# Performance work log

Hardware: AMD Instinct MI355X
Metric: run time of the kernel (lower is better)

Reference implementation:

```python
import jax, jax.numpy as jnp
import numpy as np

B, L = 4096, 200
G_DIM, L_DIM, A_DIM, H = 64, 64, 8, 32
MAX_ACTION = 1.0


def _init(k, shape, fan_in):
    bound = 1.0 / np.sqrt(fan_in)
    return jax.random.uniform(k, shape, jnp.float32, -bound, bound)


def setup_inputs() -> dict:
    key = jax.random.key(0)
    ks = jax.random.split(key, 16)
    return dict(
        global_states=jax.random.normal(ks[0], (B, G_DIM), jnp.float32),
        local_states=jax.random.normal(ks[1], (B, L, L_DIM), jnp.float32),
        W_w=_init(ks[2], (H, G_DIM), G_DIM), W_b=_init(ks[3], (H,), G_DIM),
        U_w=_init(ks[4], (H, L_DIM), L_DIM), U_b=_init(ks[5], (H,), L_DIM),
        att_w=_init(ks[6], (1, 2 * H), 2 * H), att_b=_init(ks[7], (1,), 2 * H),
        l1_w=_init(ks[8], (256, 2 * H), 2 * H), l1_b=_init(ks[9], (256,), 2 * H),
        l2_w=_init(ks[10], (256, 256), 256), l2_b=_init(ks[11], (256,), 256),
        l3_w=_init(ks[12], (A_DIM, 256), 256), l3_b=_init(ks[13], (A_DIM,), 256),
    )


def reference(global_states, local_states, W_w, W_b, U_w, U_b,
              att_w, att_b, l1_w, l1_b, l2_w, l2_b, l3_w, l3_b):
    h = W_w.shape[0]  # 32
    wg = global_states @ W_w.T + W_b                              # [B,H]
    ul = jnp.einsum('bld,hd->blh', local_states, U_w) + U_b       # [B,L,H]
    # att input row0 = cat(wg, wg); rows 1..L = cat(wg, ul)
    a_g, a_l = att_w[0, :h], att_w[0, h:]
    g_term = wg @ a_g                                             # [B]
    s0 = jax.nn.leaky_relu(g_term + wg @ a_l + att_b[0])          # [B]
    sl = jax.nn.leaky_relu(g_term[:, None] + ul @ a_l + att_b[0]) # [B,L]
    # normalize by sum (not softmax), matching torch.div(score, score.sum())
    total = s0 + sl.sum(axis=1)                                   # [B]
    n0 = s0 / total                                               # [B]
    nl = sl / total[:, None]                                      # [B,L]
    agg_local = jnp.einsum('bl,blh->bh', nl, ul)                  # [B,H]
    states = jax.nn.relu(jnp.concatenate([n0[:, None] * wg, agg_local], axis=1))  # [B,2H]
    a = jax.nn.relu(states @ l1_w.T + l1_b)
    a = jax.nn.relu(a @ l2_w.T + l2_b)
    a = jax.nn.sigmoid(a @ l3_w.T + l3_b)
    return MAX_ACTION * a
```

## Files before the change

kernel.cpp:

```cpp
#include <hip/hip_runtime.h>
#include <math.h>

#define BB 4096
#define LL 200
#define HH 32
#define PF 8

__global__ __launch_bounds__(256) void actor_fused_kernel(
    const float* __restrict__ gs,
    const float* __restrict__ ls,
    const float* __restrict__ W_w, const float* __restrict__ W_b,
    const float* __restrict__ U_w, const float* __restrict__ U_b,
    const float* __restrict__ att_w, const float* __restrict__ att_b,
    const float* __restrict__ l1_w, const float* __restrict__ l1_b,
    const float* __restrict__ l2_w, const float* __restrict__ l2_b,
    const float* __restrict__ l3_w, const float* __restrict__ l3_b,
    float* __restrict__ out)
{
    __shared__ float c_lds[4 * 64];
    __shared__ float y_lds[4 * 64];
    __shared__ __align__(16) float s_x [4 * 64];
    __shared__ __align__(16) float s_a1[4 * 256];
    __shared__ __align__(16) float s_a2[4 * 260];

    const int tid  = threadIdx.x;
    const int lane = tid & 63;
    const int wid  = tid >> 6;
    const int b    = blockIdx.x * 4 + wid;

    const int h    = lane & 31;
    const int half = lane >> 5;
    const int q    = lane & 15;
    const int lg   = lane >> 4;


    const float4* g4 = (const float4*)(gs + (size_t)b * 64);
    const float4* W4 = (const float4*)(W_w);
    float wg = (half == 0) ? W_b[h] : 0.f;
    #pragma unroll
    for (int dd = 0; dd < 8; ++dd) {
        float4 gv = g4[half * 8 + dd];
        float4 wv = W4[h * 16 + half * 8 + dd];
        wg += gv.x * wv.x + gv.y * wv.y + gv.z * wv.z + gv.w * wv.w;
    }
    wg += __shfl_xor(wg, 32);

    float gt = wg * att_w[h];
    float t2 = wg * att_w[HH + h];
    #pragma unroll
    for (int m = 1; m < 32; m <<= 1) {
        gt += __shfl_xor(gt, m);
        t2 += __shfl_xor(t2, m);
    }
    const float attb = att_b[0];
    const float lin0 = gt + t2 + attb;
    const float s0   = (lin0 > 0.f) ? lin0 : 0.01f * lin0;

    float c = 0.f;
    float ubal = 0.f;
    #pragma unroll
    for (int hh = 0; hh < HH; ++hh) {
        const float alh = att_w[HH + hh];
        c    += alh * U_w[hh * 64 + lane];
        ubal += alh * U_b[hh];
    }
    c_lds[wid * 64 + lane] = c;
    __syncthreads();
    const float4 cq = *(const float4*)&c_lds[wid * 64 + 4 * q];
    const float base = gt + ubal + attb;

    const float4* xs = (const float4*)(ls + (size_t)b * (LL * 64));
    const int idx0 = lg * 16 + q;
    float4 yx = make_float4(0.f, 0.f, 0.f, 0.f);
    float Sacc = 0.f;

    float4 Xbuf[PF];
    #pragma unroll
    for (int i = 0; i < PF; ++i)
        Xbuf[i] = xs[idx0 + i * 64];

    #pragma unroll
    for (int t = 0; t < 50; ++t) {
        float4 X = Xbuf[t & (PF - 1)];
        int tn = t + PF;
        if (tn > 49) tn = 49;
        Xbuf[t & (PF - 1)] = xs[idx0 + tn * 64];

        float p = X.x * cq.x + X.y * cq.y + X.z * cq.z + X.w * cq.w;
        p += __shfl_xor(p, 1);
        p += __shfl_xor(p, 2);
        p += __shfl_xor(p, 4);
        p += __shfl_xor(p, 8);
        const float linv = p + base;
        const float sl = (linv > 0.f) ? linv : 0.01f * linv;
        yx.x += sl * X.x;
        yx.y += sl * X.y;
        yx.z += sl * X.z;
        yx.w += sl * X.w;
        Sacc += sl;
    }

    #pragma unroll
    for (int m = 16; m < 64; m <<= 1) {
        yx.x += __shfl_xor(yx.x, m);
        yx.y += __shfl_xor(yx.y, m);
        yx.z += __shfl_xor(yx.z, m);
        yx.w += __shfl_xor(yx.w, m);
        Sacc += __shfl_xor(Sacc, m);
    }
    if (lane < 16) *(float4*)&y_lds[wid * 64 + 4 * q] = yx;
    __syncthreads();

    float V = (half == 0) ? (U_b[h] * Sacc) : 0.f;
    const float4* U4 = (const float4*)U_w;
    const float4* y4 = (const float4*)&y_lds[wid * 64];
    #pragma unroll
    for (int dd = 0; dd < 8; ++dd) {
        float4 uv = U4[h * 16 + half * 8 + dd];
        float4 yv = y4[half * 8 + dd];
        V += uv.x * yv.x + uv.y * yv.y + uv.z * yv.z + uv.w * yv.w;
    }
    V += __shfl_xor(V, 32);

    const float total = s0 + Sacc;
    const float n0    = s0 / total;
    const float outv  = (lane < 32) ? (n0 * wg) : (V / total);
    s_x[wid * 64 + lane] = fmaxf(outv, 0.f);
    __syncthreads();


    float w[64];

    {
        const float* wr = l1_w + tid * 64;
        #pragma unroll
        for (int d = 0; d < 64; ++d) w[d] = wr[d];
        float bias = l1_b[tid];
        #pragma unroll
        for (int r = 0; r < 4; ++r) {
            float acc = bias;
            #pragma unroll
            for (int d = 0; d < 64; ++d)
                acc += s_x[r * 64 + d] * w[d];
            s_a1[r * 256 + tid] = fmaxf(acc, 0.f);
        }
    }
    __syncthreads();

    {
        float acc[4];
        float bias = l2_b[tid];
        #pragma unroll
        for (int r = 0; r < 4; ++r) acc[r] = bias;
        for (int kc = 0; kc < 4; ++kc) {
            const float* wr = l2_w + tid * 256 + kc * 64;
            #pragma unroll
            for (int d = 0; d < 64; ++d) w[d] = wr[d];
            #pragma unroll
            for (int r = 0; r < 4; ++r) {
                #pragma unroll
                for (int d = 0; d < 64; ++d)
                    acc[r] += s_a1[r * 256 + kc * 64 + d] * w[d];
            }
        }
        #pragma unroll
        for (int r = 0; r < 4; ++r)
            s_a2[r * 260 + tid] = fmaxf(acc[r], 0.f);
    }
    __syncthreads();

    if (tid < 32) {
        int r = tid >> 3, o = tid & 7;
        float acc = l3_b[o];
        const float4* wr4 = (const float4*)(l3_w + o * 256);
        const float4* a4  = (const float4*)&s_a2[r * 260];
        #pragma unroll 8
        for (int k = 0; k < 64; ++k) {
            float4 av = a4[k];
            float4 wv = wr4[k];
            acc += av.x * wv.x + av.y * wv.y + av.z * wv.z + av.w * wv.w;
        }
        out[(size_t)(blockIdx.x * 4 + r) * 8 + o] =
            1.f / (1.f + __expf(-acc));
    }
}

extern "C" void kernel_launch(void* const* d_in, const int* in_sizes, int n_in,
                              void* d_out, int out_size, void* d_ws, size_t ws_size,
                              hipStream_t stream)
{
    const float* gs    = (const float*)d_in[0];
    const float* ls    = (const float*)d_in[1];
    const float* W_w   = (const float*)d_in[2];
    const float* W_b   = (const float*)d_in[3];
    const float* U_w   = (const float*)d_in[4];
    const float* U_b   = (const float*)d_in[5];
    const float* att_w = (const float*)d_in[6];
    const float* att_b = (const float*)d_in[7];
    const float* l1_w  = (const float*)d_in[8];
    const float* l1_b  = (const float*)d_in[9];
    const float* l2_w  = (const float*)d_in[10];
    const float* l2_b  = (const float*)d_in[11];
    const float* l3_w  = (const float*)d_in[12];
    const float* l3_b  = (const float*)d_in[13];

    actor_fused_kernel<<<BB / 4, 256, 0, stream>>>(
        gs, ls, W_w, W_b, U_w, U_b, att_w, att_b,
        l1_w, l1_b, l2_w, l2_b, l3_w, l3_b, (float*)d_out);
}
```

Before: 354.5 us.

## Process 16 batch rows per block to amortize MLP weight loads

Each block now handles 16 batch rows with 1024 threads instead of 4 rows with 256, so each l1/l2 weight row is loaded once per 16 rows rather than per 4. This cuts cache and memory traffic for the MLP weights. The MLP stages now use float4 weight and activation loads, and the shared c vector is stored once per block. In exchange, only 256 of the 1024 threads work during the MLP stages and there are far fewer blocks, which may underfill the GPU. The larger per-thread accumulators under the tightened launch bounds may also cause register spills.

```diff
diff --git a/kernel.cpp b/kernel.cpp
--- a/kernel.cpp
+++ b/kernel.cpp
@@ -5,8 +5,10 @@
 #define LL 200
 #define HH 32
 #define PF 8
-
-__global__ __launch_bounds__(256) void actor_fused_kernel(
+#define ROWS 16
+
+
+__global__ __launch_bounds__(1024, 4) void actor_fused_kernel(
     const float* __restrict__ gs,
     const float* __restrict__ ls,
     const float* __restrict__ W_w, const float* __restrict__ W_b,
@@ -17,21 +19,20 @@
     const float* __restrict__ l3_w, const float* __restrict__ l3_b,
     float* __restrict__ out)
 {
-    __shared__ float c_lds[4 * 64];
-    __shared__ float y_lds[4 * 64];
-    __shared__ __align__(16) float s_x [4 * 64];
-    __shared__ __align__(16) float s_a1[4 * 256];
-    __shared__ __align__(16) float s_a2[4 * 260];
+    __shared__ float c_lds[64];
+    __shared__ __align__(16) float y_lds[ROWS][64];
+    __shared__ __align__(16) float s_x [ROWS * 64];
+    __shared__ __align__(16) float s_a1[ROWS * 260];
+    __shared__ __align__(16) float s_a2[ROWS * 260];
 
     const int tid  = threadIdx.x;
     const int lane = tid & 63;
     const int wid  = tid >> 6;
-    const int b    = blockIdx.x * 4 + wid;
+    const int b    = blockIdx.x * ROWS + wid;
 
     const int h    = lane & 31;
     const int half = lane >> 5;
     const int q    = lane & 15;
-    const int lg   = lane >> 4;
 
 
     const float4* g4 = (const float4*)(gs + (size_t)b * 64);
@@ -64,27 +65,26 @@
         c    += alh * U_w[hh * 64 + lane];
         ubal += alh * U_b[hh];
     }
-    c_lds[wid * 64 + lane] = c;
-    __syncthreads();
-    const float4 cq = *(const float4*)&c_lds[wid * 64 + 4 * q];
+    c_lds[lane] = c;
+    __syncthreads();
+    const float4 cq = *(const float4*)&c_lds[4 * q];
     const float base = gt + ubal + attb;
 
     const float4* xs = (const float4*)(ls + (size_t)b * (LL * 64));
-    const int idx0 = lg * 16 + q;
     float4 yx = make_float4(0.f, 0.f, 0.f, 0.f);
     float Sacc = 0.f;
 
     float4 Xbuf[PF];
     #pragma unroll
     for (int i = 0; i < PF; ++i)
-        Xbuf[i] = xs[idx0 + i * 64];
+        Xbuf[i] = xs[lane + i * 64];
 
     #pragma unroll
     for (int t = 0; t < 50; ++t) {
         float4 X = Xbuf[t & (PF - 1)];
         int tn = t + PF;
         if (tn > 49) tn = 49;
-        Xbuf[t & (PF - 1)] = xs[idx0 + tn * 64];
+        Xbuf[t & (PF - 1)] = xs[lane + tn * 64];
 
         float p = X.x * cq.x + X.y * cq.y + X.z * cq.z + X.w * cq.w;
         p += __shfl_xor(p, 1);
@@ -108,12 +108,12 @@
         yx.w += __shfl_xor(yx.w, m);
         Sacc += __shfl_xor(Sacc, m);
     }
-    if (lane < 16) *(float4*)&y_lds[wid * 64 + 4 * q] = yx;
+    if (lane < 16) *(float4*)&y_lds[wid][4 * q] = yx;
     __syncthreads();
 
     float V = (half == 0) ? (U_b[h] * Sacc) : 0.f;
     const float4* U4 = (const float4*)U_w;
-    const float4* y4 = (const float4*)&y_lds[wid * 64];
+    const float4* y4 = (const float4*)&y_lds[wid][0];
     #pragma unroll
     for (int dd = 0; dd < 8; ++dd) {
         float4 uv = U4[h * 16 + half * 8 + dd];
@@ -128,59 +128,70 @@
     s_x[wid * 64 + lane] = fmaxf(outv, 0.f);
     __syncthreads();
 
-
-    float w[64];
-
-    {
-        const float* wr = l1_w + tid * 64;
-        #pragma unroll
-        for (int d = 0; d < 64; ++d) w[d] = wr[d];
-        float bias = l1_b[tid];
-        #pragma unroll
-        for (int r = 0; r < 4; ++r) {
-            float acc = bias;
+    const int u = tid & 255;
+
+    if (tid < 256) {
+        float4 wv[16];
+        const float4* wr4 = (const float4*)(l1_w + u * 64);
+        #pragma unroll
+        for (int i = 0; i < 16; ++i) wv[i] = wr4[i];
+        float acc[ROWS];
+        const float bias = l1_b[u];
+        #pragma unroll
+        for (int r = 0; r < ROWS; ++r) acc[r] = bias;
+        #pragma unroll
+        for (int i = 0; i < 16; ++i) {
+            const float4 w4v = wv[i];
             #pragma unroll
-            for (int d = 0; d < 64; ++d)
-                acc += s_x[r * 64 + d] * w[d];
-            s_a1[r * 256 + tid] = fmaxf(acc, 0.f);
-        }
-    }
-    __syncthreads();
-
-    {
-        float acc[4];
-        float bias = l2_b[tid];
-        #pragma unroll
-        for (int r = 0; r < 4; ++r) acc[r] = bias;
-        for (int kc = 0; kc < 4; ++kc) {
-            const float* wr = l2_w + tid * 256 + kc * 64;
-            #pragma unroll
-            for (int d = 0; d < 64; ++d) w[d] = wr[d];
-            #pragma unroll
-            for (int r = 0; r < 4; ++r) {
-                #pragma unroll
-                for (int d = 0; d < 64; ++d)
-                    acc[r] += s_a1[r * 256 + kc * 64 + d] * w[d];
+            for (int r = 0; r < ROWS; ++r) {
+                const float4 xv = *(const float4*)&s_x[r * 64 + i * 4];
+                acc[r] += w4v.x * xv.x + w4v.y * xv.y + w4v.z * xv.z + w4v.w * xv.w;
             }
         }
         #pragma unroll
-        for (int r = 0; r < 4; ++r)
-            s_a2[r * 260 + tid] = fmaxf(acc[r], 0.f);
-    }
-    __syncthreads();
-
-    if (tid < 32) {
-        int r = tid >> 3, o = tid & 7;
+        for (int r = 0; r < ROWS; ++r)
+            s_a1[r * 260 + u] = fmaxf(acc[r], 0.f);
+    }
+    __syncthreads();
+
+    if (tid < 256) {
+        float acc[ROWS];
+        const float bias = l2_b[u];
+        #pragma unroll
+        for (int r = 0; r < ROWS; ++r) acc[r] = bias;
+        for (int kc = 0; kc < 4; ++kc) {
+            float4 wv[16];
+            const float4* wr4 = (const float4*)(l2_w + (size_t)u * 256 + kc * 64);
+            #pragma unroll
+            for (int i = 0; i < 16; ++i) wv[i] = wr4[i];
+            #pragma unroll
+            for (int i = 0; i < 16; ++i) {
+                const float4 w4v = wv[i];
+                #pragma unroll
+                for (int r = 0; r < ROWS; ++r) {
+                    const float4 av = *(const float4*)&s_a1[r * 260 + kc * 64 + i * 4];
+                    acc[r] += w4v.x * av.x + w4v.y * av.y + w4v.z * av.z + w4v.w * av.w;
+                }
+            }
+        }
+        #pragma unroll
+        for (int r = 0; r < ROWS; ++r)
+            s_a2[r * 260 + u] = fmaxf(acc[r], 0.f);
+    }
+    __syncthreads();
+
+    if (tid < 128) {
+        const int r = tid >> 3, o = tid & 7;
         float acc = l3_b[o];
         const float4* wr4 = (const float4*)(l3_w + o * 256);
         const float4* a4  = (const float4*)&s_a2[r * 260];
         #pragma unroll 8
         for (int k = 0; k < 64; ++k) {
             float4 av = a4[k];
-            float4 wv = wr4[k];
-            acc += av.x * wv.x + av.y * wv.y + av.z * wv.z + av.w * wv.w;
+            float4 wvv = wr4[k];
+            acc += av.x * wvv.x + av.y * wvv.y + av.z * wvv.z + av.w * wvv.w;
         }
-        out[(size_t)(blockIdx.x * 4 + r) * 8 + o] =
+        out[((size_t)blockIdx.x * ROWS + r) * 8 + o] =
             1.f / (1.f + __expf(-acc));
     }
 }
@@ -204,7 +215,7 @@
     const float* l3_w  = (const float*)d_in[12];
     const float* l3_b  = (const float*)d_in[13];
 
-    actor_fused_kernel<<<BB / 4, 256, 0, stream>>>(
+    actor_fused_kernel<<<BB / ROWS, ROWS * 64, 0, stream>>>(
         gs, ls, W_w, W_b, U_w, U_b, att_w, att_b,
         l1_w, l1_b, l2_w, l2_b, l3_w, l3_b, (float*)d_out);
 }
```

Result: slower. 401.1 us (+13.1%).
